# Performance work log

Hardware: AMD Instinct MI355X
Metric: run time of the kernel (lower is better)

The kernel has to match this reference:

```python
import jax, jax.numpy as jnp
import numpy as np
import math

H = 16
D_MODEL = 1024
D_K = 64
BS = 8
SEQ = 1024


def setup_inputs() -> dict:
    key = jax.random.key(0)
    ks = jax.random.split(key, 13)
    s = 1.0 / math.sqrt(D_MODEL)
    inp = {
        "q": jax.random.normal(ks[0], (BS, SEQ, D_MODEL), dtype=jnp.float32),
        "k": jax.random.normal(ks[1], (BS, SEQ, D_MODEL), dtype=jnp.float32),
        "v": jax.random.normal(ks[2], (BS, SEQ, D_MODEL), dtype=jnp.float32),
        "mask": jax.random.randint(ks[3], (BS, SEQ, SEQ), 0, 2, dtype=jnp.int32),
        "Wq": jax.random.normal(ks[4], (D_MODEL, D_MODEL), dtype=jnp.float32) * s,
        "bq": jax.random.normal(ks[5], (D_MODEL,), dtype=jnp.float32) * s,
        "Wk": jax.random.normal(ks[6], (D_MODEL, D_MODEL), dtype=jnp.float32) * s,
        "bk": jax.random.normal(ks[7], (D_MODEL,), dtype=jnp.float32) * s,
        "Wv": jax.random.normal(ks[8], (D_MODEL, D_MODEL), dtype=jnp.float32) * s,
        "bv": jax.random.normal(ks[9], (D_MODEL,), dtype=jnp.float32) * s,
        "Wo": jax.random.normal(ks[10], (D_MODEL, D_MODEL), dtype=jnp.float32) * s,
        "bo": jax.random.normal(ks[11], (D_MODEL,), dtype=jnp.float32) * s,
    }
    return inp


def reference(q, k, v, mask, Wq, bq, Wk, bk, Wv, bv, Wo, bo):
    bs, seq, _ = q.shape
    # projections, split heads: [b, h, s, dk]
    def proj(x, W, b):
        y = x @ W + b
        return y.reshape(bs, seq, H, D_K).transpose(0, 2, 1, 3)
    qh = proj(q, Wq, bq)
    kh = proj(k, Wk, bk)
    vh = proj(v, Wv, bv)
    # scaled dot-product attention (dropout is identity in eval mode)
    scores = jnp.einsum("bhqd,bhkd->bhqk", qh, kh) / math.sqrt(D_K)
    scores = jnp.where(mask[:, None, :, :] == 0, jnp.float32(-1e9), scores)
    attn = jax.nn.softmax(scores, axis=-1)
    ctx = jnp.einsum("bhqk,bhkd->bhqd", attn, vh)
    concat = ctx.transpose(0, 2, 1, 3).reshape(bs, seq, D_MODEL)
    return concat @ Wo + bo
```

## Files before the change

### kernel.cpp

```cpp
#include <hip/hip_runtime.h>
#include <hip/hip_bf16.h>

#define HN 16
#define DM 1024
#define DK 64
#define BSZ 8
#define SEQL 1024

typedef __attribute__((ext_vector_type(8))) short bf16x8;
typedef __attribute__((ext_vector_type(4))) short short4v;
typedef __attribute__((ext_vector_type(4))) float f32x4;

__device__ __forceinline__ short f2bf(float f) {
    union { float f; unsigned u; } x; x.f = f;
    unsigned u = x.u + 0x7FFFu + ((x.u >> 16) & 1u);
    return (short)(u >> 16);
}

__device__ __forceinline__ void async16(const short* g, short* ldsbase) {
    __builtin_amdgcn_global_load_lds(
        (const __attribute__((address_space(1))) unsigned int*)g,
        (__attribute__((address_space(3))) unsigned int*)ldsbase, 16, 0, 0);
}

__device__ __forceinline__ short4v pack4bf(float v0, float v1, float v2, float v3) {
    unsigned pk0, pk1;
    asm("v_cvt_pk_bf16_f32 %0, %1, %2" : "=v"(pk0) : "v"(v0), "v"(v1));
    asm("v_cvt_pk_bf16_f32 %0, %1, %2" : "=v"(pk1) : "v"(v2), "v"(v3));
    union { unsigned u[2]; short4v s4; } u_;
    u_.u[0] = pk0; u_.u[1] = pk1;
    return u_.s4;
}

__global__ __launch_bounds__(256) void cast_bf16(const float* __restrict__ in,
                                                 short* __restrict__ out) {
    size_t i = (size_t)blockIdx.x * 256 + threadIdx.x;
    float4 a = ((const float4*)in)[2 * i];
    float4 b = ((const float4*)in)[2 * i + 1];
    bf16x8 r = {f2bf(a.x), f2bf(a.y), f2bf(a.z), f2bf(a.w),
                f2bf(b.x), f2bf(b.y), f2bf(b.z), f2bf(b.w)};
    ((bf16x8*)out)[i] = r;
}

__global__ __launch_bounds__(256) void transpose_cast(const float* __restrict__ W,
                                                      short* __restrict__ Wt) {
    __shared__ float tile[32][33];
    const int t = threadIdx.x;
    const int k0 = blockIdx.x * 32, n0 = blockIdx.y * 32;
    const int c = t & 31, r = t >> 5;
    #pragma unroll
    for (int p = 0; p < 4; ++p)
        tile[r + 8 * p][c] = W[(size_t)(k0 + r + 8 * p) * DM + n0 + c];
    __syncthreads();
    #pragma unroll
    for (int p = 0; p < 4; ++p)
        Wt[(size_t)(n0 + r + 8 * p) * DM + k0 + c] = f2bf(tile[c][r + 8 * p]);
}

__global__ __launch_bounds__(256) void pack_mask(const int* __restrict__ mask,
                                                 unsigned long long* __restrict__ bits) {
    size_t i = (size_t)blockIdx.x * 256 + threadIdx.x;
    unsigned long long b = __ballot(mask[i] != 0);
    if ((threadIdx.x & 63) == 0) bits[i >> 6] = b;
}

template <int MODE>
__global__ __launch_bounds__(256) void gemm_mfma(const short* __restrict__ A,
                                                 const short* __restrict__ Wt,
                                                 const float* __restrict__ bias,
                                                 void* __restrict__ Cp) {
    __shared__ __attribute__((aligned(16))) short As[128][32];
    __shared__ __attribute__((aligned(16))) short Bs[128][32];
    const int t = threadIdx.x;
    const int lane = t & 63, wv = t >> 6;
    const int wm = (wv >> 1) * 64, wn = (wv & 1) * 64;
    const int quad = lane >> 4, l15 = lane & 15;
    const int tileM = blockIdx.x * 128, tileN = blockIdx.y * 128;
    const size_t zoff = (size_t)blockIdx.z * DM * SEQL;
    const short* Az = A + zoff;

    const int sr = wv * 16 + (lane >> 2);
    const int sc = (lane & 3) * 8;

    f32x4 acc[4][4];
    #pragma unroll
    for (int i = 0; i < 4; ++i)
        #pragma unroll
        for (int j = 0; j < 4; ++j) acc[i][j] = {0.f, 0.f, 0.f, 0.f};

    for (int k0 = 0; k0 < DM; k0 += 32) {
        #pragma unroll
        for (int p = 0; p < 2; ++p) {
            async16(Az + (size_t)(tileM + p * 64 + sr) * DM + k0 + sc,
                    &As[p * 64 + wv * 16][0]);
            async16(Wt + (size_t)(tileN + p * 64 + sr) * DM + k0 + sc,
                    &Bs[p * 64 + wv * 16][0]);
        }
        __syncthreads();
        bf16x8 a[4], b[4];
        #pragma unroll
        for (int i = 0; i < 4; ++i) a[i] = *(const bf16x8*)&As[wm + i * 16 + l15][quad * 8];
        #pragma unroll
        for (int j = 0; j < 4; ++j) b[j] = *(const bf16x8*)&Bs[wn + j * 16 + l15][quad * 8];
        #pragma unroll
        for (int i = 0; i < 4; ++i)
            #pragma unroll
            for (int j = 0; j < 4; ++j)
                acc[i][j] = __builtin_amdgcn_mfma_f32_16x16x32_bf16(a[i], b[j], acc[i][j], 0, 0, 0);
        __syncthreads();
    }

    if (MODE == 2) {
        short* C = (short*)Cp + zoff;
        #pragma unroll
        for (int i = 0; i < 4; ++i)
            #pragma unroll
            for (int j = 0; j < 4; ++j) {
                int rowb = tileM + wm + i * 16 + quad * 4;
                int col = tileN + wn + j * 16 + l15;
                float b = bias[col];
                short4v s4 = pack4bf(acc[i][j][0] + b, acc[i][j][1] + b,
                                     acc[i][j][2] + b, acc[i][j][3] + b);
                *(short4v*)(C + (size_t)col * SEQL + rowb) = s4;
            }
    } else {
        #pragma unroll
        for (int i = 0; i < 4; ++i)
            #pragma unroll
            for (int j = 0; j < 4; ++j)
                #pragma unroll
                for (int rr = 0; rr < 4; ++rr) {
                    int row = tileM + wm + i * 16 + quad * 4 + rr;
                    int col = tileN + wn + j * 16 + l15;
                    float v = acc[i][j][rr] + bias[col];
                    if (MODE == 0) {
                        short* C = (short*)Cp + zoff;
                        C[((size_t)(col >> 6) * SEQL + row) * DK + (col & 63)] = f2bf(v);
                    } else {
                        float* C = (float*)Cp + zoff;
                        C[(size_t)row * DM + col] = v;
                    }
                }
    }
}

template <bool USE_BITS>
__global__ __launch_bounds__(256) void attn_mfma(const short* __restrict__ Qw,
                                                 const short* __restrict__ Kw,
                                                 const short* __restrict__ Vt,
                                                 const void* __restrict__ maskp,
                                                 short* __restrict__ ctx) {
    __shared__ __attribute__((aligned(16))) short Qs[64][72];
    __shared__ __attribute__((aligned(16))) short Ks[64][72];
    __shared__ __attribute__((aligned(16))) short Vs[64][72];
    __shared__ __attribute__((aligned(16))) short Ps[4][16][72];
    const int t = threadIdx.x;
    const int lane = t & 63, w = t >> 6;
    const int quad = lane >> 4, l15 = lane & 15;
    const int nwg = gridDim.x;
    const int cpx = nwg >> 3;
    const int vb = (blockIdx.x & 7) * cpx + (blockIdx.x >> 3);
    const int q0 = (vb & 15) * 64;
    const int h = (vb >> 4) & 15;
    const int z = vb >> 8;
    const size_t zoff = (size_t)z * DM * SEQL;
    const short* Qb = Qw + zoff + (size_t)h * SEQL * DK;
    const short* Kb = Kw + zoff + (size_t)h * SEQL * DK;
    const short* Vb = Vt + zoff + (size_t)h * DK * SEQL;

    #pragma unroll
    for (int p = 0; p < 2; ++p) {
        int cc = t + 256 * p;
        int row = cc >> 3, off = (cc & 7) * 8;
        *(bf16x8*)&Qs[row][off] = *(const bf16x8*)(Qb + (size_t)(q0 + row) * DK + off);
    }

    f32x4 o[4];
    #pragma unroll
    for (int td = 0; td < 4; ++td) o[td] = {0.f, 0.f, 0.f, 0.f};
    float Lacc = 0.f;

    for (int j0 = 0; j0 < SEQL; j0 += 64) {
        #pragma unroll
        for (int p = 0; p < 2; ++p) {
            int cc = t + 256 * p;
            int row = cc >> 3, off = (cc & 7) * 8;
            *(bf16x8*)&Ks[row][off] = *(const bf16x8*)(Kb + (size_t)(j0 + row) * DK + off);
            *(bf16x8*)&Vs[row][off] = *(const bf16x8*)(Vb + (size_t)row * SEQL + j0 + off);
        }
        __syncthreads();

        unsigned long long mw = 0;
        if (USE_BITS) {
            const unsigned long long* mb =
                (const unsigned long long*)maskp + (size_t)z * SEQL * 16;
            mw = mb[(size_t)(q0 + w * 16 + l15) * 16 + (j0 >> 6)];
        }

        #pragma unroll
        for (int tn = 0; tn < 4; ++tn) {
            f32x4 s = {0.f, 0.f, 0.f, 0.f};
            #pragma unroll
            for (int ks = 0; ks < 2; ++ks) {
                bf16x8 ak = *(const bf16x8*)&Ks[tn * 16 + l15][ks * 32 + quad * 8];
                bf16x8 bq = *(const bf16x8*)&Qs[w * 16 + l15][ks * 32 + quad * 8];
                s = __builtin_amdgcn_mfma_f32_16x16x32_bf16(ak, bq, s, 0, 0, 0);
            }
            float pv[4];
            #pragma unroll
            for (int rr = 0; rr < 4; ++rr) {
                bool keep;
                if (USE_BITS) {
                    keep = (mw >> (tn * 16 + quad * 4 + rr)) & 1ull;
                } else {
                    const int* mi = (const int*)maskp + (size_t)z * SEQL * SEQL;
                    keep = mi[(size_t)(q0 + w * 16 + l15) * SEQL + j0 + tn * 16 + quad * 4 + rr] != 0;
                }
                float e = __expf(s[rr] * 0.125f);
                pv[rr] = keep ? e : 0.0f;
                Lacc += pv[rr];
            }
            *(short4v*)&Ps[w][l15][tn * 16 + quad * 4] =
                pack4bf(pv[0], pv[1], pv[2], pv[3]);
        }
        #pragma unroll
        for (int td = 0; td < 4; ++td)
            #pragma unroll
            for (int ks = 0; ks < 2; ++ks) {
                bf16x8 ap = *(const bf16x8*)&Ps[w][l15][ks * 32 + quad * 8];
                bf16x8 bv = *(const bf16x8*)&Vs[td * 16 + l15][ks * 32 + quad * 8];
                o[td] = __builtin_amdgcn_mfma_f32_16x16x32_bf16(ap, bv, o[td], 0, 0, 0);
            }
        __syncthreads();
    }

    Lacc += __shfl_xor(Lacc, 16);
    Lacc += __shfl_xor(Lacc, 32);
    float Linv = 1.0f / Lacc;
    float Linv4[4];
    #pragma unroll
    for (int rr = 0; rr < 4; ++rr)
        Linv4[rr] = __shfl(Linv, quad * 4 + rr);

    short* cb = ctx + zoff;
    #pragma unroll
    for (int td = 0; td < 4; ++td)
        #pragma unroll
        for (int rr = 0; rr < 4; ++rr) {
            int rq = q0 + w * 16 + quad * 4 + rr;
            int cd = h * 64 + td * 16 + l15;
            cb[(size_t)rq * DM + cd] = f2bf(o[td][rr] * Linv4[rr]);
        }
}

extern "C" void kernel_launch(void* const* d_in, const int* in_sizes, int n_in,
                              void* d_out, int out_size, void* d_ws, size_t ws_size,
                              hipStream_t stream) {
    const float* q  = (const float*)d_in[0];
    const float* k  = (const float*)d_in[1];
    const float* v  = (const float*)d_in[2];
    const int* mask = (const int*)d_in[3];
    const float* Wq = (const float*)d_in[4];
    const float* bq = (const float*)d_in[5];
    const float* Wk = (const float*)d_in[6];
    const float* bk = (const float*)d_in[7];
    const float* Wv = (const float*)d_in[8];
    const float* bv = (const float*)d_in[9];
    const float* Wo = (const float*)d_in[10];
    const float* bo = (const float*)d_in[11];
    float* out = (float*)d_out;

    const size_t MB = (size_t)1 << 20;
    const size_t MEL = (size_t)1024 * 1024;
    char* base = (char*)d_ws;

    short* Wqt = (short*)(base + 0 * 2 * MB);
    short* Wkt = (short*)(base + 1 * 2 * MB);
    short* Wvt = (short*)(base + 2 * 2 * MB);
    short* Wot = (short*)(base + 3 * 2 * MB);

    int zdim;
    bool use_bits;
    if      (ws_size >= 74 * MB) { zdim = 8; use_bits = true; }
    else if (ws_size >= 42 * MB) { zdim = 4; use_bits = true; }
    else if (ws_size >= 26 * MB) { zdim = 2; use_bits = true; }
    else if (ws_size >= 18 * MB) { zdim = 1; use_bits = true; }
    else                         { zdim = 1; use_bits = false; }

    unsigned long long* bits = (unsigned long long*)(base + 8 * MB);
    char* bufs = base + (use_bits ? 9 : 8) * MB;
    const size_t bufB = (size_t)zdim * 2 * MB;
    short* Qw  = (short*)(bufs);
    short* Kw  = (short*)(bufs + bufB);
    short* Vw  = (short*)(bufs + 2 * bufB);
    short* ctx = (short*)(bufs + 3 * bufB);

    transpose_cast<<<dim3(32, 32), 256, 0, stream>>>(Wq, Wqt);
    transpose_cast<<<dim3(32, 32), 256, 0, stream>>>(Wk, Wkt);
    transpose_cast<<<dim3(32, 32), 256, 0, stream>>>(Wv, Wvt);
    transpose_cast<<<dim3(32, 32), 256, 0, stream>>>(Wo, Wot);
    if (use_bits)
        pack_mask<<<(BSZ * SEQL * SEQL) / 256, 256, 0, stream>>>(mask, bits);

    const int iters = BSZ / zdim;
    for (int it = 0; it < iters; ++it) {
        const size_t boff = (size_t)it * zdim * MEL;
        const float* qb = q + boff;
        const float* kb = k + boff;
        const float* vb = v + boff;
        float* ob = out + boff;
        const void* mb = use_bits
            ? (const void*)(bits + (size_t)it * zdim * SEQL * 16)
            : (const void*)(mask + (size_t)it * zdim * SEQL * SEQL);

        const int castGrid = zdim * 512;
        cast_bf16<<<castGrid, 256, 0, stream>>>(qb, ctx);
        gemm_mfma<0><<<dim3(8, 8, zdim), 256, 0, stream>>>(ctx, Wqt, bq, Qw);
        cast_bf16<<<castGrid, 256, 0, stream>>>(kb, ctx);
        gemm_mfma<0><<<dim3(8, 8, zdim), 256, 0, stream>>>(ctx, Wkt, bk, Kw);
        cast_bf16<<<castGrid, 256, 0, stream>>>(vb, ctx);
        gemm_mfma<2><<<dim3(8, 8, zdim), 256, 0, stream>>>(ctx, Wvt, bv, Vw);

        const int attnBlocks = 16 * 16 * zdim;
        if (use_bits)
            attn_mfma<true><<<attnBlocks, 256, 0, stream>>>(Qw, Kw, Vw, mb, ctx);
        else
            attn_mfma<false><<<attnBlocks, 256, 0, stream>>>(Qw, Kw, Vw, mb, ctx);

        gemm_mfma<1><<<dim3(8, 8, zdim), 256, 0, stream>>>(ctx, Wot, bo, ob);
    }
}
```

Baseline: 396.0 us.

## Double-buffer GEMM and attention LDS loads, keep Q in registers, repack mask bits

The GEMM kernel now double-buffers its A/B tiles with async global-to-LDS loads, so the next k-slice is prefetched while MFMAs run, using explicit vmcnt waits and raw barriers. The attention kernel double-buffers its K/V tiles through async loads into XOR-swizzled LDS to avoid bank conflicts. It holds Q fragments in registers instead of LDS and preloads each row's mask bits once. The mask packer emits a permuted 16-bit layout so each lane can read its nibble directly. This trades more LDS and more complex, fragile waitcnt logic for overlap of memory latency with compute.

New measurement: 448.0 us. 13.1% more time.

```diff
diff --git a/kernel.cpp b/kernel.cpp
--- a/kernel.cpp
+++ b/kernel.cpp
@@ -10,6 +10,7 @@
 typedef __attribute__((ext_vector_type(8))) short bf16x8;
 typedef __attribute__((ext_vector_type(4))) short short4v;
 typedef __attribute__((ext_vector_type(4))) float f32x4;
+typedef __attribute__((ext_vector_type(8))) unsigned short u16x8;
 
 __device__ __forceinline__ short f2bf(float f) {
     union { float f; unsigned u; } x; x.f = f;
@@ -58,10 +59,16 @@
 }
 
 __global__ __launch_bounds__(256) void pack_mask(const int* __restrict__ mask,
-                                                 unsigned long long* __restrict__ bits) {
-    size_t i = (size_t)blockIdx.x * 256 + threadIdx.x;
-    unsigned long long b = __ballot(mask[i] != 0);
-    if ((threadIdx.x & 63) == 0) bits[i >> 6] = b;
+                                                 unsigned short* __restrict__ bt) {
+    size_t gi = (size_t)blockIdx.x * 256 + threadIdx.x;
+    size_t word = gi >> 6;
+    int l = threadIdx.x & 63;
+    int jperm = ((l >> 2) & 3) * 16 + ((l >> 4) & 3) * 4 + (l & 3);
+    size_t row = word >> 4;
+    int jblk = (int)(word & 15);
+    unsigned long long b = __ballot(mask[row * SEQL + jblk * 64 + jperm] != 0);
+    if (l < 4)
+        bt[row * 64 + l * 16 + jblk] = (unsigned short)(b >> (l * 16));
 }
 
 template <int MODE>
@@ -69,8 +76,8 @@
                                                  const short* __restrict__ Wt,
                                                  const float* __restrict__ bias,
                                                  void* __restrict__ Cp) {
-    __shared__ __attribute__((aligned(16))) short As[128][32];
-    __shared__ __attribute__((aligned(16))) short Bs[128][32];
+    __shared__ __attribute__((aligned(16))) short As[2][128][32];
+    __shared__ __attribute__((aligned(16))) short Bs[2][128][32];
     const int t = threadIdx.x;
     const int lane = t & 63, wv = t >> 6;
     const int wm = (wv >> 1) * 64, wn = (wv & 1) * 64;
@@ -81,6 +88,8 @@
 
     const int sr = wv * 16 + (lane >> 2);
     const int sc = (lane & 3) * 8;
+    const short* asrc = Az + (size_t)(tileM + sr) * DM + sc;
+    const short* bsrc = Wt + (size_t)(tileN + sr) * DM + sc;
 
     f32x4 acc[4][4];
     #pragma unroll
@@ -88,26 +97,42 @@
         #pragma unroll
         for (int j = 0; j < 4; ++j) acc[i][j] = {0.f, 0.f, 0.f, 0.f};
 
-    for (int k0 = 0; k0 < DM; k0 += 32) {
-        #pragma unroll
-        for (int p = 0; p < 2; ++p) {
-            async16(Az + (size_t)(tileM + p * 64 + sr) * DM + k0 + sc,
-                    &As[p * 64 + wv * 16][0]);
-            async16(Wt + (size_t)(tileN + p * 64 + sr) * DM + k0 + sc,
-                    &Bs[p * 64 + wv * 16][0]);
-        }
-        __syncthreads();
+    #pragma unroll
+    for (int p = 0; p < 2; ++p) {
+        async16(asrc + (size_t)p * 64 * DM, &As[0][p * 64 + wv * 16][0]);
+        async16(bsrc + (size_t)p * 64 * DM, &Bs[0][p * 64 + wv * 16][0]);
+    }
+
+    #pragma unroll 2
+    for (int idx = 0; idx < DM / 32; ++idx) {
+        const int cur = idx & 1;
+        const int k0 = idx * 32;
+        if (k0 + 32 < DM) {
+            #pragma unroll
+            for (int p = 0; p < 2; ++p) {
+                async16(asrc + (size_t)p * 64 * DM + (k0 + 32),
+                        &As[cur ^ 1][p * 64 + wv * 16][0]);
+                async16(bsrc + (size_t)p * 64 * DM + (k0 + 32),
+                        &Bs[cur ^ 1][p * 64 + wv * 16][0]);
+            }
+            asm volatile("s_waitcnt vmcnt(4)" ::: "memory");
+        } else {
+            asm volatile("s_waitcnt vmcnt(0)" ::: "memory");
+        }
+        __builtin_amdgcn_s_barrier();
+        __builtin_amdgcn_sched_barrier(0);
+
         bf16x8 a[4], b[4];
         #pragma unroll
-        for (int i = 0; i < 4; ++i) a[i] = *(const bf16x8*)&As[wm + i * 16 + l15][quad * 8];
-        #pragma unroll
-        for (int j = 0; j < 4; ++j) b[j] = *(const bf16x8*)&Bs[wn + j * 16 + l15][quad * 8];
+        for (int i = 0; i < 4; ++i) a[i] = *(const bf16x8*)&As[cur][wm + i * 16 + l15][quad * 8];
+        #pragma unroll
+        for (int j = 0; j < 4; ++j) b[j] = *(const bf16x8*)&Bs[cur][wn + j * 16 + l15][quad * 8];
         #pragma unroll
         for (int i = 0; i < 4; ++i)
             #pragma unroll
             for (int j = 0; j < 4; ++j)
                 acc[i][j] = __builtin_amdgcn_mfma_f32_16x16x32_bf16(a[i], b[j], acc[i][j], 0, 0, 0);
-        __syncthreads();
+        __builtin_amdgcn_s_barrier();
     }
 
     if (MODE == 2) {
@@ -150,10 +175,9 @@
                                                  const short* __restrict__ Vt,
                                                  const void* __restrict__ maskp,
                                                  short* __restrict__ ctx) {
-    __shared__ __attribute__((aligned(16))) short Qs[64][72];
-    __shared__ __attribute__((aligned(16))) short Ks[64][72];
-    __shared__ __attribute__((aligned(16))) short Vs[64][72];
-    __shared__ __attribute__((aligned(16))) short Ps[4][16][72];
+    __shared__ __attribute__((aligned(16))) short Kbuf[2][64 * 64];
+    __shared__ __attribute__((aligned(16))) short Vbuf[2][64 * 64];
+    __shared__ __attribute__((aligned(16))) short Ps[4][16 * 64];
     const int t = threadIdx.x;
     const int lane = t & 63, w = t >> 6;
     const int quad = lane >> 4, l15 = lane & 15;
@@ -167,12 +191,39 @@
     const short* Qb = Qw + zoff + (size_t)h * SEQL * DK;
     const short* Kb = Kw + zoff + (size_t)h * SEQL * DK;
     const short* Vb = Vt + zoff + (size_t)h * DK * SEQL;
-
+    const int qrow = q0 + w * 16 + l15;
+    const int x = (l15 & 7) << 3;
+
+    bf16x8 qf0 = *(const bf16x8*)(Qb + (size_t)qrow * DK + quad * 8);
+    bf16x8 qf1 = *(const bf16x8*)(Qb + (size_t)qrow * DK + 32 + quad * 8);
+
+    u16x8 mv0 = {0, 0, 0, 0, 0, 0, 0, 0}, mv1 = {0, 0, 0, 0, 0, 0, 0, 0};
+    if (USE_BITS) {
+        const unsigned short* bt = (const unsigned short*)maskp +
+            (size_t)z * SEQL * 64 + (size_t)qrow * 64 + quad * 16;
+        mv0 = *(const u16x8*)bt;
+        mv1 = *(const u16x8*)(bt + 8);
+    }
+
+    const int r0 = t >> 3;
+    const int c16 = t & 7;
+    const short* ksrc[2];
+    const short* vsrc[2];
     #pragma unroll
     for (int p = 0; p < 2; ++p) {
-        int cc = t + 256 * p;
-        int row = cc >> 3, off = (cc & 7) * 8;
-        *(bf16x8*)&Qs[row][off] = *(const bf16x8*)(Qb + (size_t)(q0 + row) * DK + off);
+        int row = r0 + 32 * p;
+        int kc = (c16 ^ (row & 7)) * 8;
+        ksrc[p] = Kb + (size_t)row * DK + kc;
+        vsrc[p] = Vb + (size_t)row * SEQL + kc;
+    }
+
+    asm volatile("s_waitcnt vmcnt(0)" ::: "memory");
+    __syncthreads();
+
+    #pragma unroll
+    for (int p = 0; p < 2; ++p) {
+        async16(ksrc[p], &Kbuf[0][p * 2048 + w * 512]);
+        async16(vsrc[p], &Vbuf[0][p * 2048 + w * 512]);
     }
 
     f32x4 o[4];
@@ -180,58 +231,69 @@
     for (int td = 0; td < 4; ++td) o[td] = {0.f, 0.f, 0.f, 0.f};
     float Lacc = 0.f;
 
-    for (int j0 = 0; j0 < SEQL; j0 += 64) {
-        #pragma unroll
-        for (int p = 0; p < 2; ++p) {
-            int cc = t + 256 * p;
-            int row = cc >> 3, off = (cc & 7) * 8;
-            *(bf16x8*)&Ks[row][off] = *(const bf16x8*)(Kb + (size_t)(j0 + row) * DK + off);
-            *(bf16x8*)&Vs[row][off] = *(const bf16x8*)(Vb + (size_t)row * SEQL + j0 + off);
-        }
-        __syncthreads();
-
-        unsigned long long mw = 0;
-        if (USE_BITS) {
-            const unsigned long long* mb =
-                (const unsigned long long*)maskp + (size_t)z * SEQL * 16;
-            mw = mb[(size_t)(q0 + w * 16 + l15) * 16 + (j0 >> 6)];
-        }
+    #pragma unroll
+    for (int iter = 0; iter < 16; ++iter) {
+        const int cur = iter & 1;
+        if (iter < 15) {
+            #pragma unroll
+            for (int p = 0; p < 2; ++p) {
+                async16(ksrc[p] + (size_t)(iter + 1) * 64 * DK,
+                        &Kbuf[cur ^ 1][p * 2048 + w * 512]);
+                async16(vsrc[p] + (size_t)(iter + 1) * 64,
+                        &Vbuf[cur ^ 1][p * 2048 + w * 512]);
+            }
+            if (USE_BITS)
+                asm volatile("s_waitcnt vmcnt(4)" ::: "memory");
+            else
+                asm volatile("s_waitcnt vmcnt(0)" ::: "memory");
+        } else {
+            asm volatile("s_waitcnt vmcnt(0)" ::: "memory");
+        }
+        __builtin_amdgcn_s_barrier();
+        __builtin_amdgcn_sched_barrier(0);
+
+        const short* Kl = &Kbuf[cur][0];
+        const short* Vl = &Vbuf[cur][0];
+        const unsigned mw16 =
+            USE_BITS ? (unsigned)(iter < 8 ? mv0[iter] : mv1[iter - 8]) : 0u;
 
         #pragma unroll
         for (int tn = 0; tn < 4; ++tn) {
+            const int r = tn * 16 + l15;
+            bf16x8 ak0 = *(const bf16x8*)&Kl[r * 64 + ((quad * 8) ^ x)];
+            bf16x8 ak1 = *(const bf16x8*)&Kl[r * 64 + ((32 + quad * 8) ^ x)];
             f32x4 s = {0.f, 0.f, 0.f, 0.f};
-            #pragma unroll
-            for (int ks = 0; ks < 2; ++ks) {
-                bf16x8 ak = *(const bf16x8*)&Ks[tn * 16 + l15][ks * 32 + quad * 8];
-                bf16x8 bq = *(const bf16x8*)&Qs[w * 16 + l15][ks * 32 + quad * 8];
-                s = __builtin_amdgcn_mfma_f32_16x16x32_bf16(ak, bq, s, 0, 0, 0);
-            }
+            s = __builtin_amdgcn_mfma_f32_16x16x32_bf16(ak0, qf0, s, 0, 0, 0);
+            s = __builtin_amdgcn_mfma_f32_16x16x32_bf16(ak1, qf1, s, 0, 0, 0);
             float pv[4];
+            const unsigned nib = USE_BITS ? (mw16 >> (tn * 4)) & 0xFu : 0u;
             #pragma unroll
             for (int rr = 0; rr < 4; ++rr) {
                 bool keep;
                 if (USE_BITS) {
-                    keep = (mw >> (tn * 16 + quad * 4 + rr)) & 1ull;
+                    keep = (nib >> rr) & 1u;
                 } else {
                     const int* mi = (const int*)maskp + (size_t)z * SEQL * SEQL;
-                    keep = mi[(size_t)(q0 + w * 16 + l15) * SEQL + j0 + tn * 16 + quad * 4 + rr] != 0;
+                    keep = mi[(size_t)qrow * SEQL + iter * 64 + tn * 16 + quad * 4 + rr] != 0;
                 }
                 float e = __expf(s[rr] * 0.125f);
                 pv[rr] = keep ? e : 0.0f;
                 Lacc += pv[rr];
             }
-            *(short4v*)&Ps[w][l15][tn * 16 + quad * 4] =
+            *(short4v*)&Ps[w][l15 * 64 + ((tn * 16 + quad * 4) ^ x)] =
                 pack4bf(pv[0], pv[1], pv[2], pv[3]);
         }
-        #pragma unroll
-        for (int td = 0; td < 4; ++td)
-            #pragma unroll
-            for (int ks = 0; ks < 2; ++ks) {
-                bf16x8 ap = *(const bf16x8*)&Ps[w][l15][ks * 32 + quad * 8];
-                bf16x8 bv = *(const bf16x8*)&Vs[td * 16 + l15][ks * 32 + quad * 8];
-                o[td] = __builtin_amdgcn_mfma_f32_16x16x32_bf16(ap, bv, o[td], 0, 0, 0);
-            }
-        __syncthreads();
+        bf16x8 ap0 = *(const bf16x8*)&Ps[w][l15 * 64 + ((quad * 8) ^ x)];
+        bf16x8 ap1 = *(const bf16x8*)&Ps[w][l15 * 64 + ((32 + quad * 8) ^ x)];
+        #pragma unroll
+        for (int td = 0; td < 4; ++td) {
+            const int r = td * 16 + l15;
+            bf16x8 bv0 = *(const bf16x8*)&Vl[r * 64 + ((quad * 8) ^ x)];
+            bf16x8 bv1 = *(const bf16x8*)&Vl[r * 64 + ((32 + quad * 8) ^ x)];
+            o[td] = __builtin_amdgcn_mfma_f32_16x16x32_bf16(ap0, bv0, o[td], 0, 0, 0);
+            o[td] = __builtin_amdgcn_mfma_f32_16x16x32_bf16(ap1, bv1, o[td], 0, 0, 0);
+        }
+        __builtin_amdgcn_s_barrier();
     }
 
     Lacc += __shfl_xor(Lacc, 16);
@@ -287,7 +349,7 @@
     else if (ws_size >= 18 * MB) { zdim = 1; use_bits = true; }
     else                         { zdim = 1; use_bits = false; }
 
-    unsigned long long* bits = (unsigned long long*)(base + 8 * MB);
+    unsigned short* bits = (unsigned short*)(base + 8 * MB);
     char* bufs = base + (use_bits ? 9 : 8) * MB;
     const size_t bufB = (size_t)zdim * 2 * MB;
     short* Qw  = (short*)(bufs);
@@ -310,7 +372,7 @@
         const float* vb = v + boff;
         float* ob = out + boff;
         const void* mb = use_bits
-            ? (const void*)(bits + (size_t)it * zdim * SEQL * 16)
+            ? (const void*)(bits + (size_t)it * zdim * SEQL * 64)
             : (const void*)(mask + (size_t)it * zdim * SEQL * SEQL);
 
         const int castGrid = zdim * 512;
```
